# Kernel tuning notes

Hardware: AMD Instinct MI355X
Metric: run time of the kernel (lower is better)

Reference implementation:

```python
import jax, jax.numpy as jnp
import numpy as np

B, D, C = 8192, 1024, 8  # batch, input_size, n_conditions


def setup_inputs() -> dict:
    key = jax.random.key(0)
    k1, k2, k3, k4 = jax.random.split(key, 4)
    x = jax.random.normal(k1, (B, D), dtype=jnp.float32)
    condition_ids = jax.random.randint(k2, (B,), 0, C)  # metadata[batch_key] codes
    # Per-condition Linear(D, D) weights (torch layout: [out, in]) and biases
    W = jax.random.normal(k3, (C, D, D), dtype=jnp.float32) / np.sqrt(D)
    b = jax.random.normal(k4, (C, D), dtype=jnp.float32) * 0.01
    return {"x": x, "condition_ids": condition_ids, "W": W, "b": b}


def reference(x, condition_ids, W, b):
    # Original: for each condition c, zero non-member rows of x, apply
    # Linear_c to the FULL batch, then sum partials. Because Linear is
    # affine, the summed result per row is:
    #   out[i] = W[c_i] @ x[i] + sum_c b_c
    # (each bias b_c is added to EVERY row since the Linear runs on the
    #  full masked batch). We keep the dense per-condition GEMM structure.
    onehot = jax.nn.one_hot(condition_ids, C, dtype=x.dtype)  # [B, C]
    y = jnp.einsum('bi,coi->cbo', x, W)                       # [C, B, D]
    out = jnp.einsum('cbo,bc->bo', y, onehot) + b.sum(axis=0)  # [B, D]
    return out
```

## Files before the change

### kernel.cpp

```cpp
#include <hip/hip_runtime.h>
#include <hip/hip_bf16.h>
#include <cstdint>

#define B_ROWS 8192
#define DIM    1024
#define NC     8
#define NXCD   8
#define SLOTS  8
#define BM     256
#define BN     256

typedef __bf16 bf16;
typedef __bf16 bf16x4 __attribute__((ext_vector_type(4)));
typedef __bf16 bf16x8 __attribute__((ext_vector_type(8)));
typedef float  f32x4  __attribute__((ext_vector_type(4)));

typedef __attribute__((address_space(3))) void* lds_vp;
typedef const __attribute__((address_space(1))) void* gbl_vp;

#define XF4 (B_ROWS * DIM / 4)
__global__ __launch_bounds__(1024) void prep_kernel(
    const float* __restrict__ x, const float* __restrict__ W,
    const int* __restrict__ ids, const float* __restrict__ b,
    bf16* __restrict__ xb, bf16* __restrict__ wb,
    int* __restrict__ row_list, int* __restrict__ xmeta,
    float* __restrict__ bias_sum) {
    if (blockIdx.x != 0) {
        size_t base = (size_t)(blockIdx.x - 1) * 8192 + threadIdx.x;
        const float4* src;
        bf16* dst;
        if (base < (size_t)XF4) { src = (const float4*)x; dst = xb; }
        else                    { src = (const float4*)W; dst = wb; base -= (size_t)XF4; }
        float4 v[8];
#pragma unroll
        for (int k = 0; k < 8; k++) v[k] = src[base + (size_t)k * 1024];
#pragma unroll
        for (int k = 0; k < 8; k++) {
            bf16x4 o;
            o[0] = (bf16)v[k].x; o[1] = (bf16)v[k].y;
            o[2] = (bf16)v[k].z; o[3] = (bf16)v[k].w;
            *(bf16x4*)(dst + 4 * (base + (size_t)k * 1024)) = o;
        }
        return;
    }
    __shared__ int wtot_s[16][NC];
    __shared__ int cnt_s[NC];
    __shared__ int off_s[NC];
    __shared__ int used_s[NXCD];
    __shared__ int novf_s[NC];
    int tid = threadIdx.x, lane = tid & 63, wv = tid >> 6;
    const int per = B_ROWS / 1024;
    int base = tid * per;

    if (tid < NXCD * SLOTS) xmeta[tid * 3 + 2] = 0;

    const int4* idv = (const int4*)(ids + base);
    int4 v0 = idv[0], v1 = idv[1];
    int myid[8] = {v0.x, v0.y, v0.z, v0.w, v1.x, v1.y, v1.z, v1.w};
    unsigned long long p0 = 0, p1 = 0;
#pragma unroll
    for (int q = 0; q < 8; q++) {
        int id = myid[q];
        unsigned long long one = 1ull << ((id & 3) << 4);
        if (id < 4) p0 += one; else p1 += one;
    }
    unsigned long long i0 = p0, i1 = p1;
#pragma unroll
    for (int d = 1; d < 64; d <<= 1) {
        unsigned long long u0 = __shfl_up(i0, d, 64);
        unsigned long long u1 = __shfl_up(i1, d, 64);
        if (lane >= d) { i0 += u0; i1 += u1; }
    }
    unsigned long long e0 = i0 - p0, e1 = i1 - p1;
    unsigned long long t0 = __shfl(i0, 63, 64), t1 = __shfl(i1, 63, 64);
    if (lane == 0) {
#pragma unroll
        for (int c = 0; c < 4; c++) {
            wtot_s[wv][c]     = (int)((t0 >> (c << 4)) & 0xFFFF);
            wtot_s[wv][c + 4] = (int)((t1 >> (c << 4)) & 0xFFFF);
        }
    }
    __syncthreads();
    if (tid < NC) {
        int acc = 0;
        for (int w2 = 0; w2 < 16; w2++) { int t = wtot_s[w2][tid]; wtot_s[w2][tid] = acc; acc += t; }
        cnt_s[tid] = acc;
    }
    __syncthreads();
    if (tid < NC) {
        int acc = 0;
        for (int c2 = 0; c2 < tid; c2++) acc += cnt_s[c2];
        off_s[tid] = acc;
    }
    __syncthreads();
    if (tid < 16 * NC) wtot_s[tid >> 3][tid & 7] += off_s[tid & 7];
    __syncthreads();

    if (tid < NC) {
        int c = tid, n = cnt_s[c];
        int tc = (n + BM - 1) >> 8;
        int prim = tc < SLOTS ? tc : SLOTS;
        for (int t = 0; t < prim; t++) {
            int* e = xmeta + (c * SLOTS + t) * 3;
            int rc = n - t * BM; if (rc > BM) rc = BM;
            e[0] = c; e[1] = off_s[c] + t * BM; e[2] = rc;
        }
        used_s[c] = prim;
        novf_s[c] = tc - prim;
    }
    {
        float s = 0.f;
#pragma unroll
        for (int c = 0; c < NC; c++) s += b[c * DIM + tid];
        bias_sum[tid] = s;
    }
    __syncthreads();

    if (tid == 0) {
        int k = 0;
        for (int c = 0; c < NC; c++) {
            for (int t = 0; t < novf_s[c]; t++) {
                for (;;) {
                    int xx = k >> 3, s = k & (SLOTS - 1); k++;
                    if (s >= used_s[xx]) {
                        int* e = xmeta + (xx * SLOTS + s) * 3;
                        int rc = cnt_s[c] - (SLOTS + t) * BM; if (rc > BM) rc = BM;
                        e[0] = c; e[1] = off_s[c] + (SLOTS + t) * BM; e[2] = rc;
                        break;
                    }
                }
            }
        }
    }
    unsigned long long r0 = 0, r1 = 0;
#pragma unroll
    for (int j = 0; j < per; j++) {
        int id = myid[j];
        int sh = (id & 3) << 4;
        unsigned long long run = (id < 4) ? r0 : r1;
        unsigned long long exc = (id < 4) ? e0 : e1;
        int p = wtot_s[wv][id] + (int)((exc >> sh) & 0xFFFF) + (int)((run >> sh) & 0xFFFF);
        row_list[p] = base + j;
        unsigned long long one = 1ull << sh;
        if (id < 4) r0 += one; else r1 += one;
    }
}

#define ASZ (BM * 64)
__global__ __launch_bounds__(512, 2) void gemm_kernel(
    const bf16* __restrict__ xb, const bf16* __restrict__ wb,
    const float* __restrict__ bias_sum, const int* __restrict__ row_list,
    const int* __restrict__ xmeta, float* __restrict__ out) {
    int xcd = blockIdx.x, slot = blockIdx.y, colt = blockIdx.z;
    const int* e = xmeta + (xcd * SLOTS + slot) * 3;
    int cond = e[0], rstart = e[1], rcnt = e[2];
    if (rcnt == 0) return;
    int col0 = colt * BN;

    __shared__ bf16 lds[2][(BM + BN) * 64];

    int tid  = threadIdx.x;
    int lane = tid & 63;
    int w    = tid >> 6;
    int wr   = w >> 2;
    int wc   = w & 3;
    int srow = lane >> 3;
    int scol = ((lane & 7) ^ srow) * 8;

    const bf16 *aS[4], *bS[4];
#pragma unroll
    for (int i = 0; i < 4; i++) {
        int tr = i * 64 + w * 8 + srow;
        int rr = (tr < rcnt) ? tr : 0;
        int grow = row_list[rstart + rr];
        aS[i] = xb + (size_t)grow * DIM + scol;
    }
#pragma unroll
    for (int i = 0; i < 4; i++) {
        int br = i * 64 + w * 8 + srow;
        bS[i] = wb + (size_t)cond * DIM * DIM + (size_t)(col0 + br) * DIM + scol;
    }

    f32x4 acc[8][4];
#pragma unroll
    for (int m = 0; m < 8; m++)
#pragma unroll
        for (int n = 0; n < 4; n++) acc[m][n] = (f32x4){0.f, 0.f, 0.f, 0.f};

    int fr = lane & 15;
    int fq = lane >> 4;
    int off0 = (fq * 16) ^ ((fr & 7) << 4);
    int off1 = off0 ^ 64;

    auto stage = [&](int buf, int k0) {
#pragma unroll
        for (int i = 0; i < 4; i++)
            __builtin_amdgcn_global_load_lds((gbl_vp)(aS[i] + k0),
                                             (lds_vp)(&lds[buf][(i * 64 + w * 8) * 64]),
                                             16, 0, 0);
#pragma unroll
        for (int i = 0; i < 4; i++)
            __builtin_amdgcn_global_load_lds((gbl_vp)(bS[i] + k0),
                                             (lds_vp)(&lds[buf][ASZ + (i * 64 + w * 8) * 64]),
                                             16, 0, 0);
    };

    stage(0, 0);
    stage(1, 64);

    const int NT = DIM / 64;
    for (int t = 0; t < NT; ++t) {
        if (t < NT - 1) asm volatile("s_waitcnt vmcnt(8)" ::: "memory");
        else            asm volatile("s_waitcnt vmcnt(0)" ::: "memory");
        __builtin_amdgcn_s_barrier();

        const char* baseA = (const char*)&lds[t & 1][0] + (wr * 128 + fr) * 128;
        const char* baseB = (const char*)&lds[t & 1][0] + ASZ * 2 + (wc * 64 + fr) * 128;
#pragma unroll
        for (int kk = 0; kk < 2; ++kk) {
            int ofs = kk ? off1 : off0;
            bf16x8 af[8], bv[4];
#pragma unroll
            for (int m = 0; m < 8; m++) af[m] = *(const bf16x8*)(baseA + m * 2048 + ofs);
#pragma unroll
            for (int n = 0; n < 4; n++) bv[n] = *(const bf16x8*)(baseB + n * 2048 + ofs);
            __builtin_amdgcn_s_setprio(1);
#pragma unroll
            for (int m = 0; m < 8; m++)
#pragma unroll
                for (int n = 0; n < 4; n++)
                    acc[m][n] = __builtin_amdgcn_mfma_f32_16x16x32_bf16(
                        af[m], bv[n], acc[m][n], 0, 0, 0);
            __builtin_amdgcn_s_setprio(0);
        }

        asm volatile("s_waitcnt lgkmcnt(0)" ::: "memory");
        __builtin_amdgcn_s_barrier();
        if (t + 2 < NT) stage(t & 1, (t + 2) * 64);
    }

    float bias[4];
#pragma unroll
    for (int n = 0; n < 4; n++) bias[n] = bias_sum[col0 + wc * 64 + n * 16 + fr];
#pragma unroll
    for (int m = 0; m < 8; m++) {
#pragma unroll
        for (int i = 0; i < 4; i++) {
            int rl = wr * 128 + m * 16 + fq * 4 + i;
            if (rl < rcnt) {
                int grow = row_list[rstart + rl];
                float* op = out + (size_t)grow * DIM + col0 + wc * 64 + fr;
#pragma unroll
                for (int n = 0; n < 4; n++) op[n * 16] = acc[m][n][i] + bias[n];
            }
        }
    }
}

__global__ void naive_kernel(const float* __restrict__ x, const int* __restrict__ ids,
                             const float* __restrict__ W, const float* __restrict__ b,
                             float* __restrict__ out) {
    int row = blockIdx.x;
    int c = ids[row];
    __shared__ float xs[DIM];
    for (int i = threadIdx.x; i < DIM; i += 256) xs[i] = x[(size_t)row * DIM + i];
    __syncthreads();
    const float* Wc = W + (size_t)c * DIM * DIM;
    for (int o = threadIdx.x; o < DIM; o += 256) {
        float s = 0.f;
        const float* wrp = Wc + (size_t)o * DIM;
        for (int i = 0; i < DIM; i++) s += xs[i] * wrp[i];
        float bs = 0.f;
#pragma unroll
        for (int cc = 0; cc < NC; cc++) bs += b[cc * DIM + o];
        out[(size_t)row * DIM + o] = s + bs;
    }
}

extern "C" void kernel_launch(void* const* d_in, const int* in_sizes, int n_in,
                              void* d_out, int out_size, void* d_ws, size_t ws_size,
                              hipStream_t stream) {
    const float* x   = (const float*)d_in[0];
    const int*   ids = (const int*)d_in[1];
    const float* W   = (const float*)d_in[2];
    const float* b   = (const float*)d_in[3];
    float*       out = (float*)d_out;

    size_t xb_off   = 0;
    size_t xb_sz    = (size_t)B_ROWS * DIM * 2;
    size_t wb_off   = (xb_off + xb_sz + 255) & ~(size_t)255;
    size_t wb_sz    = (size_t)NC * DIM * DIM * 2;
    size_t bias_off = (wb_off + wb_sz + 255) & ~(size_t)255;
    size_t rl_off   = (bias_off + DIM * 4 + 255) & ~(size_t)255;
    size_t meta_off = (rl_off + B_ROWS * 4 + 255) & ~(size_t)255;
    size_t need     = meta_off + (size_t)NXCD * SLOTS * 3 * 4;

    if (ws_size < need) {
        naive_kernel<<<dim3(B_ROWS), dim3(256), 0, stream>>>(x, ids, W, b, out);
        return;
    }

    char* ws = (char*)d_ws;
    bf16*  xb       = (bf16*)(ws + xb_off);
    bf16*  wbf      = (bf16*)(ws + wb_off);
    float* bias_sum = (float*)(ws + bias_off);
    int*   row_list = (int*)(ws + rl_off);
    int*   xmeta    = (int*)(ws + meta_off);

    prep_kernel<<<dim3(513), dim3(1024), 0, stream>>>(x, W, ids, b, xb, wbf,
                                                      row_list, xmeta, bias_sum);
    gemm_kernel<<<dim3(NXCD, SLOTS, DIM / BN), dim3(512), 0, stream>>>(
        xb, wbf, bias_sum, row_list, xmeta, out);
}
```

Before: 58.61 us.

## Shrink N tile to 128 and use triple-buffered LDS with interleaved staging

Halves the column tile to 128 and rearranges the 8 waves as 4x2, each computing 64x64. LDS goes from double to triple buffering, and global-to-LDS loads for stage t+2 are spread across four MFMA phases per k-step, separated by barriers. Waves whose row block lies beyond the segment's row count skip their MFMAs. The intent is better overlap of loads with compute and more blocks for load balance, at the cost of more barriers, lower per-block reuse of x, and possibly higher LDS pressure that limits occupancy (144KB per block).

```diff
diff --git a/kernel.cpp b/kernel.cpp
--- a/kernel.cpp
+++ b/kernel.cpp
@@ -8,7 +8,8 @@
 #define NXCD   8
 #define SLOTS  8
 #define BM     256
-#define BN     256
+#define BN     128
+#define NT     16
 
 typedef __bf16 bf16;
 typedef __bf16 bf16x4 __attribute__((ext_vector_type(4)));
@@ -146,7 +147,8 @@
     }
 }
 
-#define ASZ (BM * 64)
+#define BUFB   49152
+#define ABYTES 32768
 __global__ __launch_bounds__(512, 2) void gemm_kernel(
     const bf16* __restrict__ xb, const bf16* __restrict__ wb,
     const float* __restrict__ bias_sum, const int* __restrict__ row_list,
@@ -157,17 +159,17 @@
     if (rcnt == 0) return;
     int col0 = colt * BN;
 
-    __shared__ bf16 lds[2][(BM + BN) * 64];
+    __shared__ char lds[3 * BUFB];
 
     int tid  = threadIdx.x;
     int lane = tid & 63;
     int w    = tid >> 6;
-    int wr   = w >> 2;
-    int wc   = w & 3;
+    int wr   = w >> 1;
+    int wc   = w & 1;
     int srow = lane >> 3;
     int scol = ((lane & 7) ^ srow) * 8;
 
-    const bf16 *aS[4], *bS[4];
+    const bf16 *aS[4], *bS[2];
 #pragma unroll
     for (int i = 0; i < 4; i++) {
         int tr = i * 64 + w * 8 + srow;
@@ -176,14 +178,14 @@
         aS[i] = xb + (size_t)grow * DIM + scol;
     }
 #pragma unroll
-    for (int i = 0; i < 4; i++) {
+    for (int i = 0; i < 2; i++) {
         int br = i * 64 + w * 8 + srow;
         bS[i] = wb + (size_t)cond * DIM * DIM + (size_t)(col0 + br) * DIM + scol;
     }
 
-    f32x4 acc[8][4];
-#pragma unroll
-    for (int m = 0; m < 8; m++)
+    f32x4 acc[4][4];
+#pragma unroll
+    for (int m = 0; m < 4; m++)
 #pragma unroll
         for (int n = 0; n < 4; n++) acc[m][n] = (f32x4){0.f, 0.f, 0.f, 0.f};
 
@@ -191,62 +193,114 @@
     int fq = lane >> 4;
     int off0 = (fq * 16) ^ ((fr & 7) << 4);
     int off1 = off0 ^ 64;
-
-    auto stage = [&](int buf, int k0) {
-#pragma unroll
-        for (int i = 0; i < 4; i++)
-            __builtin_amdgcn_global_load_lds((gbl_vp)(aS[i] + k0),
-                                             (lds_vp)(&lds[buf][(i * 64 + w * 8) * 64]),
-                                             16, 0, 0);
-#pragma unroll
-        for (int i = 0; i < 4; i++)
-            __builtin_amdgcn_global_load_lds((gbl_vp)(bS[i] + k0),
-                                             (lds_vp)(&lds[buf][ASZ + (i * 64 + w * 8) * 64]),
-                                             16, 0, 0);
+    bool mAct = (wr * 64) < rcnt;
+
+    auto stgA = [&](int buf, int k0, int i) {
+        __builtin_amdgcn_global_load_lds((gbl_vp)(aS[i] + k0),
+            (lds_vp)(lds + buf * BUFB + (i * 64 + w * 8) * 128), 16, 0, 0);
     };
-
-    stage(0, 0);
-    stage(1, 64);
-
-    const int NT = DIM / 64;
+    auto stgB = [&](int buf, int k0, int i) {
+        __builtin_amdgcn_global_load_lds((gbl_vp)(bS[i] + k0),
+            (lds_vp)(lds + buf * BUFB + ABYTES + (i * 64 + w * 8) * 128), 16, 0, 0);
+    };
+
+#pragma unroll
+    for (int i = 0; i < 4; i++) stgA(0, 0, i);
+#pragma unroll
+    for (int i = 0; i < 2; i++) stgB(0, 0, i);
+#pragma unroll
+    for (int i = 0; i < 4; i++) stgA(1, 64, i);
+#pragma unroll
+    for (int i = 0; i < 2; i++) stgB(1, 64, i);
+    asm volatile("s_waitcnt vmcnt(6)" ::: "memory");
+    __builtin_amdgcn_s_barrier();
+
     for (int t = 0; t < NT; ++t) {
-        if (t < NT - 1) asm volatile("s_waitcnt vmcnt(8)" ::: "memory");
-        else            asm volatile("s_waitcnt vmcnt(0)" ::: "memory");
-        __builtin_amdgcn_s_barrier();
-
-        const char* baseA = (const char*)&lds[t & 1][0] + (wr * 128 + fr) * 128;
-        const char* baseB = (const char*)&lds[t & 1][0] + ASZ * 2 + (wc * 64 + fr) * 128;
-#pragma unroll
-        for (int kk = 0; kk < 2; ++kk) {
-            int ofs = kk ? off1 : off0;
-            bf16x8 af[8], bv[4];
-#pragma unroll
-            for (int m = 0; m < 8; m++) af[m] = *(const bf16x8*)(baseA + m * 2048 + ofs);
-#pragma unroll
-            for (int n = 0; n < 4; n++) bv[n] = *(const bf16x8*)(baseB + n * 2048 + ofs);
-            __builtin_amdgcn_s_setprio(1);
-#pragma unroll
-            for (int m = 0; m < 8; m++)
-#pragma unroll
-                for (int n = 0; n < 4; n++)
-                    acc[m][n] = __builtin_amdgcn_mfma_f32_16x16x32_bf16(
-                        af[m], bv[n], acc[m][n], 0, 0, 0);
-            __builtin_amdgcn_s_setprio(0);
-        }
-
+        int cur = t % 3, nxt = (t + 2) % 3, k2 = (t + 2) * 64;
+        bool doStage = (t + 2) < NT;
+        const char* bA = lds + cur * BUFB + (wr * 64 + fr) * 128;
+        const char* bB = lds + cur * BUFB + ABYTES + (wc * 64 + fr) * 128;
+        bf16x8 af0, af1, bv[4];
+
+        if (mAct) { af0 = *(const bf16x8*)(bA + 0 * 2048 + off0);
+                    af1 = *(const bf16x8*)(bA + 1 * 2048 + off0); }
+#pragma unroll
+        for (int n = 0; n < 4; n++) bv[n] = *(const bf16x8*)(bB + n * 2048 + off0);
+        if (doStage) { stgA(nxt, k2, 0); stgA(nxt, k2, 1); }
+        __builtin_amdgcn_s_barrier();
         asm volatile("s_waitcnt lgkmcnt(0)" ::: "memory");
-        __builtin_amdgcn_s_barrier();
-        if (t + 2 < NT) stage(t & 1, (t + 2) * 64);
+        __builtin_amdgcn_s_setprio(1);
+        if (mAct) {
+#pragma unroll
+            for (int n = 0; n < 4; n++) {
+                acc[0][n] = __builtin_amdgcn_mfma_f32_16x16x32_bf16(af0, bv[n], acc[0][n], 0, 0, 0);
+                acc[1][n] = __builtin_amdgcn_mfma_f32_16x16x32_bf16(af1, bv[n], acc[1][n], 0, 0, 0);
+            }
+        }
+        __builtin_amdgcn_s_setprio(0);
+        __builtin_amdgcn_s_barrier();
+
+        if (mAct) { af0 = *(const bf16x8*)(bA + 2 * 2048 + off0);
+                    af1 = *(const bf16x8*)(bA + 3 * 2048 + off0); }
+        if (doStage) { stgA(nxt, k2, 2); stgA(nxt, k2, 3); }
+        __builtin_amdgcn_s_barrier();
+        asm volatile("s_waitcnt lgkmcnt(0)" ::: "memory");
+        __builtin_amdgcn_s_setprio(1);
+        if (mAct) {
+#pragma unroll
+            for (int n = 0; n < 4; n++) {
+                acc[2][n] = __builtin_amdgcn_mfma_f32_16x16x32_bf16(af0, bv[n], acc[2][n], 0, 0, 0);
+                acc[3][n] = __builtin_amdgcn_mfma_f32_16x16x32_bf16(af1, bv[n], acc[3][n], 0, 0, 0);
+            }
+        }
+        __builtin_amdgcn_s_setprio(0);
+        __builtin_amdgcn_s_barrier();
+
+        if (mAct) { af0 = *(const bf16x8*)(bA + 0 * 2048 + off1);
+                    af1 = *(const bf16x8*)(bA + 1 * 2048 + off1); }
+#pragma unroll
+        for (int n = 0; n < 4; n++) bv[n] = *(const bf16x8*)(bB + n * 2048 + off1);
+        if (doStage) stgB(nxt, k2, 0);
+        __builtin_amdgcn_s_barrier();
+        asm volatile("s_waitcnt lgkmcnt(0)" ::: "memory");
+        __builtin_amdgcn_s_setprio(1);
+        if (mAct) {
+#pragma unroll
+            for (int n = 0; n < 4; n++) {
+                acc[0][n] = __builtin_amdgcn_mfma_f32_16x16x32_bf16(af0, bv[n], acc[0][n], 0, 0, 0);
+                acc[1][n] = __builtin_amdgcn_mfma_f32_16x16x32_bf16(af1, bv[n], acc[1][n], 0, 0, 0);
+            }
+        }
+        __builtin_amdgcn_s_setprio(0);
+        __builtin_amdgcn_s_barrier();
+
+        if (mAct) { af0 = *(const bf16x8*)(bA + 2 * 2048 + off1);
+                    af1 = *(const bf16x8*)(bA + 3 * 2048 + off1); }
+        if (doStage) stgB(nxt, k2, 1);
+        __builtin_amdgcn_s_barrier();
+        asm volatile("s_waitcnt lgkmcnt(0)" ::: "memory");
+        __builtin_amdgcn_s_setprio(1);
+        if (mAct) {
+#pragma unroll
+            for (int n = 0; n < 4; n++) {
+                acc[2][n] = __builtin_amdgcn_mfma_f32_16x16x32_bf16(af0, bv[n], acc[2][n], 0, 0, 0);
+                acc[3][n] = __builtin_amdgcn_mfma_f32_16x16x32_bf16(af1, bv[n], acc[3][n], 0, 0, 0);
+            }
+        }
+        __builtin_amdgcn_s_setprio(0);
+        if (t < NT - 2)       asm volatile("s_waitcnt vmcnt(6)" ::: "memory");
+        else if (t == NT - 2) asm volatile("s_waitcnt vmcnt(0)" ::: "memory");
+        __builtin_amdgcn_s_barrier();
     }
 
     float bias[4];
 #pragma unroll
     for (int n = 0; n < 4; n++) bias[n] = bias_sum[col0 + wc * 64 + n * 16 + fr];
 #pragma unroll
-    for (int m = 0; m < 8; m++) {
+    for (int m = 0; m < 4; m++) {
 #pragma unroll
         for (int i = 0; i < 4; i++) {
-            int rl = wr * 128 + m * 16 + fq * 4 + i;
+            int rl = wr * 64 + m * 16 + fq * 4 + i;
             if (rl < rcnt) {
                 int grow = row_list[rstart + rl];
                 float* op = out + (size_t)grow * DIM + col0 + wc * 64 + fr;
```

Result: slower. 66.87 us (+14.1%).
